# Kernel tuning notes

Measured on AMD Instinct MI355X. Metric: run time of the kernel, lower is better.

Reference implementation:

```python
import jax, jax.numpy as jnp
import numpy as np

B, T, STEPS = 4096, 56, 28
H, ANN, ENC, DEC = 126, 30, 20, 15
DIN = 1 + DEC + H  # decoder GRU input width = 142


def _gru_step(h, x, Wih, Whh, bih, bhh):
    # torch GRU cell math; Wih: [3H, in], Whh: [3H, H]
    gi = x @ Wih.T + bih
    gh = h @ Whh.T + bhh
    ir, iz, inn = jnp.split(gi, 3, axis=-1)
    hr, hz, hn = jnp.split(gh, 3, axis=-1)
    r = jax.nn.sigmoid(ir + hr)
    z = jax.nn.sigmoid(iz + hz)
    n = jnp.tanh(inn + r * hn)
    return (1.0 - z) * n + z * h


def setup_inputs() -> dict:
    key = jax.random.key(0)
    ks = jax.random.split(key, 23)
    p = lambda k, s: jax.random.normal(k, s, dtype=jnp.float32) * 0.08
    return {
        "ann_data": jax.random.normal(ks[0], (B, ANN), dtype=jnp.float32),
        "encoder_data": jax.random.normal(ks[1], (T, B, ENC), dtype=jnp.float32),
        "decoder_data": jax.random.normal(ks[2], (STEPS, B, DEC), dtype=jnp.float32),
        "s2h_W1": p(ks[3], (96, ANN)), "s2h_b1": p(ks[4], (96,)),
        "s2h_W2": p(ks[5], (H, 96)), "s2h_b2": p(ks[6], (H,)),
        "enc_Wih": p(ks[7], (3 * H, ENC)), "enc_Whh": p(ks[8], (3 * H, H)),
        "enc_bih": p(ks[9], (3 * H,)), "enc_bhh": p(ks[10], (3 * H,)),
        "dec_Wih": p(ks[11], (3 * H, DIN)), "dec_Whh": p(ks[12], (3 * H, H)),
        "dec_bih": p(ks[13], (3 * H,)), "dec_bhh": p(ks[14], (3 * H,)),
        "U_W": p(ks[15], (H, H)), "U_b": p(ks[16], (H,)),
        "Wl_W": p(ks[17], (H, H)), "Wl_b": p(ks[18], (H,)),
        "V_W": p(ks[19], (1, H)), "V_b": p(ks[20], (1,)),
        "h2o_W": p(ks[21], (1, H)), "h2o_b": p(ks[22], (1,)),
    }


def reference(ann_data, encoder_data, decoder_data,
              s2h_W1, s2h_b1, s2h_W2, s2h_b2,
              enc_Wih, enc_Whh, enc_bih, enc_bhh,
              dec_Wih, dec_Whh, dec_bih, dec_bhh,
              U_W, U_b, Wl_W, Wl_b, V_W, V_b, h2o_W, h2o_b):
    # static -> initial hidden: Linear(ANN,96) -> ReLU -> Linear(96,H)
    hidden = jnp.maximum(ann_data @ s2h_W1.T + s2h_b1, 0.0) @ s2h_W2.T + s2h_b2  # [B,H]

    def enc_f(h, x):
        h2 = _gru_step(h, x, enc_Wih, enc_Whh, enc_bih, enc_bhh)
        return h2, h2

    hidden, enc_out = jax.lax.scan(enc_f, hidden, encoder_data)  # enc_out: [T,B,H]

    Uo = enc_out @ U_W.T + U_b            # [T,B,H] precomputed (loop-invariant)
    gt0 = encoder_data[-1, :, 0:1]        # initial_ground, [B,1]

    def dec_f(carry, dec_x):
        h, prev = carry
        Wh = h @ Wl_W.T + Wl_b                              # [B,H]
        scores = jnp.tanh(Uo + Wh[None]) @ V_W.T + V_b      # [T,B,1]
        alpha = jax.nn.softmax(scores, axis=0)              # softmax over time
        attn = jnp.einsum('tb,tbh->bh', alpha[..., 0], enc_out)
        x = jnp.concatenate([prev, dec_x, attn], axis=1)    # [B,DIN]
        h2 = _gru_step(h, x, dec_Wih, dec_Whh, dec_bih, dec_bhh)
        out = h2 @ h2o_W.T + h2o_b                          # [B,1]
        return (h2, out), out

    _, outputs = jax.lax.scan(dec_f, (hidden, gt0), decoder_data)
    return outputs  # [STEPS, B, 1]
```

## Files before the change

kernel.cpp:

```cpp
#include <hip/hip_runtime.h>
#include <stdint.h>

typedef unsigned int u32;
typedef unsigned short u16;
typedef _Float16 f16;
typedef _Float16 f16x8 __attribute__((ext_vector_type(8)));
typedef _Float16 f16x4 __attribute__((ext_vector_type(4)));
typedef _Float16 f16x2 __attribute__((ext_vector_type(2)));
typedef float f32x4 __attribute__((ext_vector_type(4)));

constexpr int NB = 4096;
constexpr int NT = 56;
constexpr int NS = 28;
constexpr int NH = 126;
constexpr int NHP = 128;
constexpr float LOG2E = 1.4426950408889634f;

constexpr int LROW = 136;
constexpr int LB   = NT * LROW + 8;

constexpr int TJP = 120;
constexpr int TB  = 7712;

constexpr size_t OFF_H    = 0;
constexpr size_t OFF_ENC  = 2097152;
constexpr size_t OFF_UO   = OFF_ENC + 58720256;
constexpr size_t OFF_WENC = OFF_UO + 58720256;
constexpr size_t OFF_WDEC = OFF_WENC + 122880;
constexpr size_t OFF_WL   = OFF_WDEC + 221184;
constexpr size_t OFF_UW   = OFF_WL + 32768;

__device__ __forceinline__ float fexp2(float x){ return __builtin_amdgcn_exp2f(x); }
__device__ __forceinline__ float frcp (float x){ return __builtin_amdgcn_rcpf(x); }
__device__ __forceinline__ float sigm (float x){ return frcp(1.f + fexp2(-LOG2E * x)); }
__device__ __forceinline__ float ftanh(float x){ return 1.f - 2.f * frcp(1.f + fexp2(2.f * LOG2E * x)); }

__global__ void k_prep(const float* __restrict__ eWih, const float* __restrict__ eWhh,
                       const float* __restrict__ dWih, const float* __restrict__ dWhh,
                       const float* __restrict__ UW,   const float* __restrict__ Wl,
                       char* __restrict__ ws)
{
  f16* wenc = (f16*)(ws + OFF_WENC);
  f16* wdec = (f16*)(ws + OFF_WDEC);
  f16* wl   = (f16*)(ws + OFF_WL);
  f16* uw   = (f16*)(ws + OFF_UW);
  const int nE = 384 * 160, nD = 384 * 288, nW = 128 * 128;
  const int total = nE + nD + nW + nW;
  for (int i = blockIdx.x * 256 + threadIdx.x; i < total; i += gridDim.x * 256) {
    int idx = i;
    if (idx < nE) {
      const int r = idx / 160, c = idx % 160;
      float v = 0.f;
      if (r < 378) {
        if (c < 20) v = eWih[r * 20 + c];
        else if (c >= 32 && c < 158) v = eWhh[r * 126 + (c - 32)];
      }
      wenc[idx] = (f16)v; continue;
    }
    idx -= nE;
    if (idx < nD) {
      const int r = idx / 288, c = idx % 288;
      float v = 0.f;
      if (r < 378) {
        if (c < 16) v = dWih[r * 142 + c];
        else if (c >= 32 && c < 158) v = dWih[r * 142 + 16 + (c - 32)];
        else if (c >= 160 && c < 286) v = dWhh[r * 126 + (c - 160)];
      }
      wdec[idx] = (f16)v; continue;
    }
    idx -= nD;
    if (idx < nW) {
      const int r = idx >> 7, c = idx & 127;
      wl[idx] = (f16)((r < 126 && c < 126) ? Wl[r * 126 + c] : 0.f);
      continue;
    }
    idx -= nW;
    { const int r = idx >> 7, c = idx & 127;
      uw[idx] = (f16)((r < 126 && c < 126) ? UW[r * 126 + c] : 0.f); }
  }
}

__global__ __launch_bounds__(256) void k_mlp(
    const float* __restrict__ ann, const float* __restrict__ W1, const float* __restrict__ b1,
    const float* __restrict__ W2, const float* __restrict__ b2, float* __restrict__ hstate)
{
  __shared__ float anns[32][33];
  __shared__ float t1s[32][101];
  const int tid = threadIdx.x;
  const int b0 = blockIdx.x * 32;
  for (int i = tid; i < 32 * 30; i += 256)
    anns[i / 30][i % 30] = ann[(b0 + i / 30) * 30 + (i % 30)];
  __syncthreads();
  const int b = tid & 31, rg = tid >> 5;
  for (int m = rg; m < 96; m += 8) {
    float a = b1[m];
    for (int k = 0; k < 30; ++k) a += W1[m * 30 + k] * anns[b][k];
    t1s[b][m] = fmaxf(a, 0.f);
  }
  __syncthreads();
  for (int j = rg; j < NHP; j += 8) {
    float a = 0.f;
    if (j < NH) {
      a = b2[j];
      for (int k = 0; k < 96; ++k) a += W2[j * 96 + k] * t1s[b][k];
    }
    hstate[(b0 + b) * NHP + j] = a;
  }
}

__global__ __launch_bounds__(512) void k_enc(
    const float* __restrict__ xenc, const f16* __restrict__ Wenc,
    const f16* __restrict__ Uw,
    const float* __restrict__ bih, const float* __restrict__ bhh,
    const float* __restrict__ Ub,
    float* __restrict__ hstate, f16* __restrict__ encO, u16* __restrict__ uoO)
{
  __shared__ f16 av[16][296];
  const int tid = threadIdx.x;
  const int wid = tid >> 6, l = tid & 63, quad = l >> 4, col = l & 15;
  const int b0 = blockIdx.x * 16;
  const int jb = wid * 16, j = jb + col;
  const bool valid = j < NH;
  const int jc = valid ? j : NH - 1;

  const float br  = bih[jc]        + bhh[jc];
  const float bz  = bih[NH + jc]   + bhh[NH + jc];
  const float bnx = bih[2*NH + jc];
  const float bnh = bhh[2*NH + jc];
  const float ub  = Ub[jc];

  f16x8 rB[5], zB[5], nxB, nhB[4], uB[4];
  {
    const int ko = quad * 8, rr = jb + col;
#pragma unroll
    for (int kt = 0; kt < 5; ++kt) {
      rB[kt] = *(const f16x8*)&Wenc[rr * 160 + kt * 32 + ko];
      zB[kt] = *(const f16x8*)&Wenc[(NH + rr) * 160 + kt * 32 + ko];
    }
    nxB = *(const f16x8*)&Wenc[(2*NH + rr) * 160 + ko];
#pragma unroll
    for (int kt = 0; kt < 4; ++kt) {
      nhB[kt] = *(const f16x8*)&Wenc[(2*NH + rr) * 160 + 32 + kt * 32 + ko];
      uB[kt]  = *(const f16x8*)&Uw[rr * 128 + kt * 32 + ko];
    }
  }

  {
    const int bb = tid >> 5, c4 = (tid & 31) * 4;
    const float4 hv = *(const float4*)&hstate[(b0 + bb) * NHP + c4];
    av[bb][32 + c4]     = (f16)hv.x; av[bb][32 + c4 + 1] = (f16)hv.y;
    av[bb][32 + c4 + 2] = (f16)hv.z; av[bb][32 + c4 + 3] = (f16)hv.w;
  }
  if (tid < 192) { const int bb = tid / 12, p = tid % 12; av[bb][20 + p] = (f16)0.f; }
  __syncthreads();

  const int m = col, ko = quad * 8;
  for (int t = 0; t < NT; ++t) {
    const int hp = 32 + (t & 1) * 128, hq = 32 + ((t + 1) & 1) * 128;
    if (tid < 320) {
      const int bb = tid / 20, e = tid % 20;
      av[bb][e] = (f16)xenc[((size_t)t * NB + b0 + bb) * 20 + e];
    }
    __syncthreads();
    f16x8 A[5];
    A[0] = *(const f16x8*)&av[m][ko];
#pragma unroll
    for (int kt = 1; kt < 5; ++kt) A[kt] = *(const f16x8*)&av[m][hp + (kt - 1) * 32 + ko];

    f32x4 Cr = {br, br, br, br}, Cz = {bz, bz, bz, bz};
    f32x4 Cnx = {bnx, bnx, bnx, bnx}, Cnh = {bnh, bnh, bnh, bnh};
#pragma unroll
    for (int kt = 0; kt < 5; ++kt) {
      Cr = __builtin_amdgcn_mfma_f32_16x16x32_f16(A[kt], rB[kt], Cr, 0, 0, 0);
      Cz = __builtin_amdgcn_mfma_f32_16x16x32_f16(A[kt], zB[kt], Cz, 0, 0, 0);
    }
    Cnx = __builtin_amdgcn_mfma_f32_16x16x32_f16(A[0], nxB, Cnx, 0, 0, 0);
#pragma unroll
    for (int kt = 0; kt < 4; ++kt)
      Cnh = __builtin_amdgcn_mfma_f32_16x16x32_f16(A[kt + 1], nhB[kt], Cnh, 0, 0, 0);

    float hv4[4];
#pragma unroll
    for (int c = 0; c < 4; ++c) {
      const int bb = quad * 4 + c;
      const float hold = (float)av[bb][hp + j];
      const float r = sigm(Cr[c]), z = sigm(Cz[c]);
      const float n = ftanh(Cnx[c] + r * Cnh[c]);
      hv4[c] = (1.f - z) * n + z * hold;
    }
#pragma unroll
    for (int c = 0; c < 4; ++c) {
      const int bb = quad * 4 + c;
      const f16 hs = valid ? (f16)hv4[c] : (f16)0.f;
      av[bb][hq + j] = hs;
      encO[((size_t)(b0 + bb) * NT + t) * 128 + j] = hs;
    }
    if (t == NT - 1 && valid) {
#pragma unroll
      for (int c = 0; c < 4; ++c)
        hstate[(b0 + quad * 4 + c) * NHP + j] = hv4[c];
    }
    __syncthreads();

    f16x8 Ah[4];
#pragma unroll
    for (int kt = 0; kt < 4; ++kt) Ah[kt] = *(const f16x8*)&av[m][hq + kt * 32 + ko];
    f32x4 Cu = {ub, ub, ub, ub};
#pragma unroll
    for (int kt = 0; kt < 4; ++kt)
      Cu = __builtin_amdgcn_mfma_f32_16x16x32_f16(Ah[kt], uB[kt], Cu, 0, 0, 0);
#pragma unroll
    for (int c = 0; c < 4; ++c) {
      union { f16 h; u16 u; } cv;
      cv.h = (f16)fexp2(2.f * LOG2E * Cu[c]);
      uoO[((size_t)(b0 + quad * 4 + c) * NT + t) * 128 + j] = valid ? cv.u : (u16)0;
    }
  }
}

__global__ __launch_bounds__(512, 2) void k_dec(
    const float* __restrict__ xdec, const float* __restrict__ xenc,
    const f16* __restrict__ Wdec, const f16* __restrict__ WlW,
    const float* __restrict__ bih, const float* __restrict__ bhh,
    const float* __restrict__ Wlb, const float* __restrict__ Vw,
    const float* __restrict__ Vb, const float* __restrict__ how,
    const float* __restrict__ hob, const float* __restrict__ hstate,
    const f16* __restrict__ encO, const u16* __restrict__ uoO,
    float* __restrict__ out)
{
  __shared__ __align__(16) u16 uoL[4 * LB];
  __shared__ __align__(16) f16 encT[4 * TB];
  __shared__ __align__(16) f16 av[5][424];
  __shared__ float EWS[4][132];
  __shared__ float scS[4][60];
  __shared__ __align__(16) f16 hows16[128];
  const int tid = threadIdx.x;
  const int wid = tid >> 6, l = tid & 63, quad = l >> 4, col = l & 15;
  const int b0 = blockIdx.x * 4;
  const int jb = wid * 16, j = jb + col;
  const bool valid = j < NH;
  const int jc = valid ? j : NH - 1;

  const float br  = bih[jc]        + bhh[jc];
  const float bz  = bih[NH + jc]   + bhh[NH + jc];
  const float bnx = bih[2*NH + jc];
  const float bnh = bhh[2*NH + jc];
  const float wb  = Wlb[jc];
  const float vb0 = Vb[0], hob0 = hob[0];

  f16x8 rB[9], zB[9], nxB[5], nhB[4], wlB[4];
  {
    const int ko = quad * 8, rr = jb + col;
#pragma unroll
    for (int kt = 0; kt < 9; ++kt) {
      rB[kt] = *(const f16x8*)&Wdec[rr * 288 + kt * 32 + ko];
      zB[kt] = *(const f16x8*)&Wdec[(NH + rr) * 288 + kt * 32 + ko];
    }
#pragma unroll
    for (int kt = 0; kt < 5; ++kt)
      nxB[kt] = *(const f16x8*)&Wdec[(2*NH + rr) * 288 + kt * 32 + ko];
#pragma unroll
    for (int kt = 0; kt < 4; ++kt) {
      nhB[kt] = *(const f16x8*)&Wdec[(2*NH + rr) * 288 + 160 + kt * 32 + ko];
      wlB[kt] = *(const f16x8*)&WlW[rr * 128 + kt * 32 + ko];
    }
  }

  const int g = tid >> 3, sub = tid & 7;
  float n2v[16], svsum = 0.f;
#pragma unroll
  for (int i = 0; i < 16; ++i) {
    const int jj = sub * 16 + i;
    const float v = (jj < NH) ? Vw[jj] : 0.f;
    n2v[i] = -2.f * v;
    svsum += v;
  }
  if (tid >= 256 && tid < 384) {
    const int q = tid - 256; hows16[q] = (f16)((q < NH) ? how[q] : 0.f);
  }
  for (int i = tid; i < 5 * 424; i += 512) av[i / 424][i % 424] = (f16)0.f;
  if (tid < 24) EWS[tid / 6][126 + tid % 6] = 0.f;
  {
    const size_t gb = (size_t)b0 * NT * 128;
    for (int i = tid; i < 4 * NT * 16; i += 512) {
      const int ch = i & 15, btr = i >> 4;
      const int bb = btr / NT, tt = btr % NT;
      const size_t src = gb + (size_t)btr * 128 + ch * 8;
      *(f16x8*)&uoL[bb * LB + tt * LROW + ch * 8] = *(const f16x8*)&uoO[src];
      const f16x8 ev = *(const f16x8*)&encO[src];
#pragma unroll
      for (int k2 = 0; k2 < 4; ++k2) {
        f16x2 pr; pr[0] = ev[2 * k2]; pr[1] = ev[2 * k2 + 1];
        *(f16x2*)&encT[bb * TB + (ch * 4 + k2) * TJP + tt * 2] = pr;
      }
    }
  }
  __syncthreads();
  if (tid < 128) {
    const int bb = tid >> 5, c4 = (tid & 31) * 4;
    const float4 hv = *(const float4*)&hstate[(b0 + bb) * NHP + c4];
    av[bb][160 + c4]     = (f16)hv.x; av[bb][160 + c4 + 1] = (f16)hv.y;
    av[bb][160 + c4 + 2] = (f16)hv.z; av[bb][160 + c4 + 3] = (f16)hv.w;
  }
  if (tid < 4) av[tid][0] = (f16)xenc[((size_t)(NT - 1) * NB + b0 + tid) * 20];
  __syncthreads();

  const int m = col, ko = quad * 8;
  const int arow = ((m & 3) == 0) ? (m >> 2) : 4;
  const int pb = tid & 3, pth = (tid >> 2) & 1, pjp = tid >> 3;

  for (int s = 0; s < NS; ++s) {
    const int hp = 160 + (s & 1) * 128, hq = 160 + ((s + 1) & 1) * 128;

    {
      f16x8 Ah[4];
#pragma unroll
      for (int kt = 0; kt < 4; ++kt) Ah[kt] = *(const f16x8*)&av[arow][hp + kt * 32 + ko];
      f32x4 Cw = {wb, wb, wb, wb};
#pragma unroll
      for (int kt = 0; kt < 4; ++kt)
        Cw = __builtin_amdgcn_mfma_f32_16x16x32_f16(Ah[kt], wlB[kt], Cw, 0, 0, 0);
      if (valid) EWS[quad][j] = fexp2(2.f * LOG2E * Cw[0]);
      if (wid == 0 && s > 0) {
        f16x8 hB[4];
        const f16x8 zz = {};
#pragma unroll
        for (int kt = 0; kt < 4; ++kt)
          hB[kt] = (col == 0) ? *(const f16x8*)&hows16[kt * 32 + ko] : zz;
        f32x4 Co = {0.f, 0.f, 0.f, 0.f};
#pragma unroll
        for (int kt = 0; kt < 4; ++kt)
          Co = __builtin_amdgcn_mfma_f32_16x16x32_f16(Ah[kt], hB[kt], Co, 0, 0, 0);
        if (col == 0) {
          const float o = Co[0] + hob0;
          out[(size_t)(s - 1) * NB + b0 + quad] = o;
          av[quad][0] = (f16)o;
        }
      }
    }
    if (tid < 60) { const int bb = tid / 15, e = tid % 15;
      av[bb][1 + e] = (f16)xdec[((size_t)s * NB + b0 + bb) * 15 + e]; }
    __syncthreads();

    {
      const int sbb = g & 3, tb = g >> 2;
      float ew[16];
#pragma unroll
      for (int i = 0; i < 4; ++i)
        *(float4*)&ew[i * 4] = *(const float4*)&EWS[sbb][sub * 16 + i * 4];
      const u16* up0 = &uoL[sbb * LB + sub * 16];
      uint4 q0 = *(const uint4*)&up0[tb * LROW];
      uint4 q1 = *(const uint4*)&up0[tb * LROW + 8];
      float rs[4];
#pragma unroll
      for (int rd = 0; rd < 4; ++rd) {
        const int t = rd * 16 + tb;
        const u32 wsv[8] = {q0.x, q0.y, q0.z, q0.w, q1.x, q1.y, q1.z, q1.w};
        if (rd < 3) {
          const int tn = (t + 16 < NT) ? (t + 16) : (NT - 1);
          q0 = *(const uint4*)&up0[tn * LROW];
          q1 = *(const uint4*)&up0[tn * LROW + 8];
        }
        float ac0 = 0.f, ac1 = 0.f, ac2 = 0.f, ac3 = 0.f;
#pragma unroll
        for (int k = 0; k < 8; k += 2) {
          union { u32 i; f16x2 h; } ua, ub2;
          ua.i = wsv[k]; ub2.i = wsv[k + 1];
          const float p0 = fmaf((float)ua.h[0],  ew[2 * k],     1.f);
          const float p1 = fmaf((float)ua.h[1],  ew[2 * k + 1], 1.f);
          const float p2 = fmaf((float)ub2.h[0], ew[2 * k + 2], 1.f);
          const float p3 = fmaf((float)ub2.h[1], ew[2 * k + 3], 1.f);
          ac0 = fmaf(n2v[2 * k],     frcp(p0), ac0);
          ac1 = fmaf(n2v[2 * k + 1], frcp(p1), ac1);
          ac2 = fmaf(n2v[2 * k + 2], frcp(p2), ac2);
          ac3 = fmaf(n2v[2 * k + 3], frcp(p3), ac3);
        }
        rs[rd] = svsum + (ac0 + ac1) + (ac2 + ac3);
      }
      rs[0] += __shfl_xor(rs[0], 1, 64);
      rs[1] += __shfl_xor(rs[1], 1, 64);
      rs[2] += __shfl_xor(rs[2], 1, 64);
      rs[3] += __shfl_xor(rs[3], 1, 64);
      rs[0] += __shfl_xor(rs[0], 2, 64);
      rs[1] += __shfl_xor(rs[1], 2, 64);
      rs[2] += __shfl_xor(rs[2], 2, 64);
      rs[3] += __shfl_xor(rs[3], 2, 64);
      rs[0] += __shfl_xor(rs[0], 4, 64);
      rs[1] += __shfl_xor(rs[1], 4, 64);
      rs[2] += __shfl_xor(rs[2], 4, 64);
      rs[3] += __shfl_xor(rs[3], 4, 64);
      if (sub == 0) {
#pragma unroll
        for (int rd = 0; rd < 4; ++rd) {
          const int t = rd * 16 + tb;
          if (t < NT) scS[sbb][t] = fexp2(LOG2E * (rs[rd] + vb0));
        }
      }
    }
    __syncthreads();

    {
      const int j0 = pjp * 2;
      const f16* er = &encT[pb * TB + pjp * TJP + pth * 56];
      const float* scp = &scS[pb][pth * 28];
      float Za = 0.f, Zb = 0.f;
      float a0a = 0.f, a0b = 0.f, a1a = 0.f, a1b = 0.f;
#pragma unroll
      for (int it = 0; it < 7; ++it) {
        const f16x8 ev = *(const f16x8*)&er[it * 8];
        const float4 sc = *(const float4*)&scp[it * 4];
        Za += sc.x; Zb += sc.y; Za += sc.z; Zb += sc.w;
        a0a = fmaf(sc.x, (float)ev[0], a0a);
        a1a = fmaf(sc.x, (float)ev[1], a1a);
        a0b = fmaf(sc.y, (float)ev[2], a0b);
        a1b = fmaf(sc.y, (float)ev[3], a1b);
        a0a = fmaf(sc.z, (float)ev[4], a0a);
        a1a = fmaf(sc.z, (float)ev[5], a1a);
        a0b = fmaf(sc.w, (float)ev[6], a0b);
        a1b = fmaf(sc.w, (float)ev[7], a1b);
      }
      float Z = Za + Zb, a0 = a0a + a0b, a1 = a1a + a1b;
      a0 += __shfl_xor(a0, 4, 64);
      a1 += __shfl_xor(a1, 4, 64);
      Z  += __shfl_xor(Z, 4, 64);
      if (pth == 0) {
        const float inv = frcp(Z);
        f16x2 st; st[0] = (f16)(a0 * inv); st[1] = (f16)(a1 * inv);
        *(f16x2*)&av[pb][32 + j0] = st;
      }
    }
    __syncthreads();

    {
      f16x8 A[9];
#pragma unroll
      for (int kt = 0; kt < 5; ++kt) A[kt] = *(const f16x8*)&av[arow][kt * 32 + ko];
#pragma unroll
      for (int kt = 5; kt < 9; ++kt) A[kt] = *(const f16x8*)&av[arow][hp + (kt - 5) * 32 + ko];
      f32x4 Cr = {br, br, br, br}, Cz = {bz, bz, bz, bz};
      f32x4 Cnx = {bnx, bnx, bnx, bnx}, Cnh = {bnh, bnh, bnh, bnh};
#pragma unroll
      for (int kt = 0; kt < 9; ++kt) {
        Cr = __builtin_amdgcn_mfma_f32_16x16x32_f16(A[kt], rB[kt], Cr, 0, 0, 0);
        Cz = __builtin_amdgcn_mfma_f32_16x16x32_f16(A[kt], zB[kt], Cz, 0, 0, 0);
      }
#pragma unroll
      for (int kt = 0; kt < 5; ++kt)
        Cnx = __builtin_amdgcn_mfma_f32_16x16x32_f16(A[kt], nxB[kt], Cnx, 0, 0, 0);
#pragma unroll
      for (int kt = 0; kt < 4; ++kt)
        Cnh = __builtin_amdgcn_mfma_f32_16x16x32_f16(A[kt + 5], nhB[kt], Cnh, 0, 0, 0);
      {
        const float hold = (float)av[quad][hp + j];
        const float r = sigm(Cr[0]), z = sigm(Cz[0]);
        const float n = ftanh(Cnx[0] + r * Cnh[0]);
        const float h2 = (1.f - z) * n + z * hold;
        if (valid) av[quad][hq + j] = (f16)h2;
      }
    }
    __syncthreads();
  }

  if (wid == 0) {
    const int hql = 160 + (NS & 1) * 128;
    f16x8 Ah2[4], hB[4];
    const f16x8 zz = {};
#pragma unroll
    for (int kt = 0; kt < 4; ++kt) {
      Ah2[kt] = *(const f16x8*)&av[arow][hql + kt * 32 + ko];
      hB[kt] = (col == 0) ? *(const f16x8*)&hows16[kt * 32 + ko] : zz;
    }
    f32x4 Co = {0.f, 0.f, 0.f, 0.f};
#pragma unroll
    for (int kt = 0; kt < 4; ++kt)
      Co = __builtin_amdgcn_mfma_f32_16x16x32_f16(Ah2[kt], hB[kt], Co, 0, 0, 0);
    if (col == 0) out[(size_t)(NS - 1) * NB + b0 + quad] = Co[0] + hob0;
  }
}

extern "C" void kernel_launch(void* const* d_in, const int* in_sizes, int n_in,
                              void* d_out, int out_size, void* d_ws, size_t ws_size,
                              hipStream_t stream)
{
  const float* ann   = (const float*)d_in[0];
  const float* xenc  = (const float*)d_in[1];
  const float* xdec  = (const float*)d_in[2];
  const float* W1    = (const float*)d_in[3];
  const float* b1    = (const float*)d_in[4];
  const float* W2    = (const float*)d_in[5];
  const float* b2    = (const float*)d_in[6];
  const float* eWih  = (const float*)d_in[7];
  const float* eWhh  = (const float*)d_in[8];
  const float* ebih  = (const float*)d_in[9];
  const float* ebhh  = (const float*)d_in[10];
  const float* dWih  = (const float*)d_in[11];
  const float* dWhh  = (const float*)d_in[12];
  const float* dbih  = (const float*)d_in[13];
  const float* dbhh  = (const float*)d_in[14];
  const float* UW    = (const float*)d_in[15];
  const float* Ubias = (const float*)d_in[16];
  const float* Wl    = (const float*)d_in[17];
  const float* Wlb   = (const float*)d_in[18];
  const float* Vw    = (const float*)d_in[19];
  const float* Vb    = (const float*)d_in[20];
  const float* how   = (const float*)d_in[21];
  const float* hob   = (const float*)d_in[22];

  char* ws = (char*)d_ws;
  float* hstate = (float*)(ws + OFF_H);
  f16*   encB   = (f16*)(ws + OFF_ENC);
  u16*   uoB    = (u16*)(ws + OFF_UO);
  const f16* pWenc = (const f16*)(ws + OFF_WENC);
  const f16* pWdec = (const f16*)(ws + OFF_WDEC);
  const f16* pWl   = (const f16*)(ws + OFF_WL);
  const f16* pUW   = (const f16*)(ws + OFF_UW);

  k_prep<<<200, 256, 0, stream>>>(eWih, eWhh, dWih, dWhh, UW, Wl, ws);
  k_mlp <<<128, 256, 0, stream>>>(ann, W1, b1, W2, b2, hstate);
  k_enc <<<NB / 16, 512, 0, stream>>>(xenc, pWenc, pUW, ebih, ebhh, Ubias,
                                      hstate, encB, uoB);
  k_dec <<<NB / 4, 512, 0, stream>>>(xdec, xenc, pWdec, pWl, dbih, dbhh,
                                     Wlb, Vw, Vb, how, hob, hstate,
                                     encB, uoB, (float*)d_out);
}
```

Before: 584.7 us.

## Compute attention context with MFMA over j-major transposed encoder outputs

Replaces the scalar FMA loop that builds the attention context vector with MFMA 16x16x32 f16 instructions. Encoder outputs are stored j-major in LDS with zero-padded time columns. The softmax weights are also written as f16 so they can serve as the B operand, and the normalizer is reduced with lane shuffles. Only column 0 of each MFMA output is used, so most of the matrix work is wasted. Rounding the softmax weights to f16 costs some accuracy, and the byte-wise transposed LDS stores in the prologue may cause bank conflicts.

```diff
diff --git a/kernel.cpp b/kernel.cpp
--- a/kernel.cpp
+++ b/kernel.cpp
@@ -19,8 +19,8 @@
 constexpr int LROW = 136;
 constexpr int LB   = NT * LROW + 8;
 
-constexpr int TJP = 120;
-constexpr int TB  = 7712;
+constexpr int ETROW = 72;
+constexpr int ETB   = 128 * ETROW;
 
 constexpr size_t OFF_H    = 0;
 constexpr size_t OFF_ENC  = 2097152;
@@ -229,10 +229,11 @@
     float* __restrict__ out)
 {
   __shared__ __align__(16) u16 uoL[4 * LB];
-  __shared__ __align__(16) f16 encT[4 * TB];
+  __shared__ __align__(16) f16 encTj[4 * ETB];
   __shared__ __align__(16) f16 av[5][424];
   __shared__ float EWS[4][132];
-  __shared__ float scS[4][60];
+  __shared__ __align__(16) float scS[4][68];
+  __shared__ __align__(16) f16 scSf16[5][72];
   __shared__ __align__(16) f16 hows16[128];
   const int tid = threadIdx.x;
   const int wid = tid >> 6, l = tid & 63, quad = l >> 4, col = l & 15;
@@ -280,6 +281,13 @@
   }
   for (int i = tid; i < 5 * 424; i += 512) av[i / 424][i % 424] = (f16)0.f;
   if (tid < 24) EWS[tid / 6][126 + tid % 6] = 0.f;
+  for (int i = tid; i < 4 * 68; i += 512) (&scS[0][0])[i] = 0.f;
+  for (int i = tid; i < 5 * 72; i += 512) (&scSf16[0][0])[i] = (f16)0.f;
+  {
+    const f16x8 zz = {};
+    *(f16x8*)&encTj[tid * ETROW + 56] = zz;
+    *(f16x8*)&encTj[tid * ETROW + 64] = zz;
+  }
   {
     const size_t gb = (size_t)b0 * NT * 128;
     for (int i = tid; i < 4 * NT * 16; i += 512) {
@@ -289,10 +297,8 @@
       *(f16x8*)&uoL[bb * LB + tt * LROW + ch * 8] = *(const f16x8*)&uoO[src];
       const f16x8 ev = *(const f16x8*)&encO[src];
 #pragma unroll
-      for (int k2 = 0; k2 < 4; ++k2) {
-        f16x2 pr; pr[0] = ev[2 * k2]; pr[1] = ev[2 * k2 + 1];
-        *(f16x2*)&encT[bb * TB + (ch * 4 + k2) * TJP + tt * 2] = pr;
-      }
+      for (int k2 = 0; k2 < 8; ++k2)
+        encTj[bb * ETB + (ch * 8 + k2) * ETROW + tt] = ev[k2];
     }
   }
   __syncthreads();
@@ -307,7 +313,6 @@
 
   const int m = col, ko = quad * 8;
   const int arow = ((m & 3) == 0) ? (m >> 2) : 4;
-  const int pb = tid & 3, pth = (tid >> 2) & 1, pjp = tid >> 3;
 
   for (int s = 0; s < NS; ++s) {
     const int hp = 160 + (s & 1) * 128, hq = 160 + ((s + 1) & 1) * 128;
@@ -393,40 +398,42 @@
 #pragma unroll
         for (int rd = 0; rd < 4; ++rd) {
           const int t = rd * 16 + tb;
-          if (t < NT) scS[sbb][t] = fexp2(LOG2E * (rs[rd] + vb0));
+          if (t < NT) {
+            const float ex = fexp2(LOG2E * (rs[rd] + vb0));
+            scS[sbb][t] = ex;
+            scSf16[sbb][t] = (f16)ex;
+          }
         }
       }
     }
     __syncthreads();
 
     {
-      const int j0 = pjp * 2;
-      const f16* er = &encT[pb * TB + pjp * TJP + pth * 56];
-      const float* scp = &scS[pb][pth * 28];
-      float Za = 0.f, Zb = 0.f;
-      float a0a = 0.f, a0b = 0.f, a1a = 0.f, a1b = 0.f;
-#pragma unroll
-      for (int it = 0; it < 7; ++it) {
-        const f16x8 ev = *(const f16x8*)&er[it * 8];
-        const float4 sc = *(const float4*)&scp[it * 4];
-        Za += sc.x; Zb += sc.y; Za += sc.z; Zb += sc.w;
-        a0a = fmaf(sc.x, (float)ev[0], a0a);
-        a1a = fmaf(sc.x, (float)ev[1], a1a);
-        a0b = fmaf(sc.y, (float)ev[2], a0b);
-        a1b = fmaf(sc.y, (float)ev[3], a1b);
-        a0a = fmaf(sc.z, (float)ev[4], a0a);
-        a1a = fmaf(sc.z, (float)ev[5], a1a);
-        a0b = fmaf(sc.w, (float)ev[6], a0b);
-        a1b = fmaf(sc.w, (float)ev[7], a1b);
-      }
-      float Z = Za + Zb, a0 = a0a + a0b, a1 = a1a + a1b;
-      a0 += __shfl_xor(a0, 4, 64);
-      a1 += __shfl_xor(a1, 4, 64);
-      Z  += __shfl_xor(Z, 4, 64);
-      if (pth == 0) {
-        const float inv = frcp(Z);
-        f16x2 st; st[0] = (f16)(a0 * inv); st[1] = (f16)(a1 * inv);
-        *(f16x2*)&av[pb][32 + j0] = st;
+      const float4 zv = *(const float4*)&scS[quad][col * 4];
+      float Zp = (zv.x + zv.y) + (zv.z + zv.w);
+      Zp += __shfl_xor(Zp, 1, 64);
+      Zp += __shfl_xor(Zp, 2, 64);
+      Zp += __shfl_xor(Zp, 4, 64);
+      Zp += __shfl_xor(Zp, 8, 64);
+      const float invZq = frcp(Zp);
+#pragma unroll
+      for (int b = 0; b < 4; ++b) {
+        const float ivb = __shfl(invZq, b * 16 + col, 64);
+        const f16* ar = &encTj[b * ETB + (jb + col) * ETROW];
+        const f16x8 A0 = *(const f16x8*)&ar[ko];
+        const f16x8 A1 = *(const f16x8*)&ar[32 + ko];
+        const int rbat = (col == 0) ? b : 4;
+        const f16x8 B0 = *(const f16x8*)&scSf16[rbat][ko];
+        const f16x8 B1 = *(const f16x8*)&scSf16[rbat][32 + ko];
+        f32x4 Ca = {0.f, 0.f, 0.f, 0.f};
+        Ca = __builtin_amdgcn_mfma_f32_16x16x32_f16(A0, B0, Ca, 0, 0, 0);
+        Ca = __builtin_amdgcn_mfma_f32_16x16x32_f16(A1, B1, Ca, 0, 0, 0);
+        if (col == 0) {
+          f16x4 st;
+#pragma unroll
+          for (int r = 0; r < 4; ++r) st[r] = (f16)(Ca[r] * ivb);
+          *(f16x4*)&av[b][32 + jb + quad * 4] = st;
+        }
       }
     }
     __syncthreads();
```

Result: slower. 614.1 us (+5.0%).

## Split decoder GRU matmuls across two wave halves using 1024-thread blocks

Applied to the files above, without the earlier changes.

The decoder kernel doubles its block to 1024 threads. The two halves of the waves split the GRU gate work: one half computes the input-side projections for r, z and n, the other computes the hidden-side projections and the Wl attention query. Partial sums pass through new shared arrays with an extra barrier. The attention score and context loops are also re-split so each thread handles fewer timesteps, and n2v moves into shared memory. The goal is to shorten the serial per-step critical path and cut register pressure, at the cost of more barriers, more shared memory and possibly lower occupancy.

```diff
diff --git a/kernel.cpp b/kernel.cpp
--- a/kernel.cpp
+++ b/kernel.cpp
@@ -218,7 +218,7 @@
   }
 }
 
-__global__ __launch_bounds__(512, 2) void k_dec(
+__global__ __launch_bounds__(1024, 4) void k_dec(
     const float* __restrict__ xdec, const float* __restrict__ xenc,
     const f16* __restrict__ Wdec, const f16* __restrict__ WlW,
     const float* __restrict__ bih, const float* __restrict__ bhh,
@@ -233,11 +233,14 @@
   __shared__ __align__(16) f16 av[5][424];
   __shared__ float EWS[4][132];
   __shared__ float scS[4][60];
+  __shared__ float pxr[4][132], pxz[4][132], pxn[4][132];
+  __shared__ float n2vL[128];
   __shared__ __align__(16) f16 hows16[128];
   const int tid = threadIdx.x;
   const int wid = tid >> 6, l = tid & 63, quad = l >> 4, col = l & 15;
+  const int kh = wid >> 3, jw = wid & 7;
   const int b0 = blockIdx.x * 4;
-  const int jb = wid * 16, j = jb + col;
+  const int jb = jw * 16, j = jb + col;
   const bool valid = j < NH;
   const int jc = valid ? j : NH - 1;
 
@@ -248,41 +251,44 @@
   const float wb  = Wlb[jc];
   const float vb0 = Vb[0], hob0 = hob[0];
 
-  f16x8 rB[9], zB[9], nxB[5], nhB[4], wlB[4];
+  f16x8 W[16];
   {
     const int ko = quad * 8, rr = jb + col;
-#pragma unroll
-    for (int kt = 0; kt < 9; ++kt) {
-      rB[kt] = *(const f16x8*)&Wdec[rr * 288 + kt * 32 + ko];
-      zB[kt] = *(const f16x8*)&Wdec[(NH + rr) * 288 + kt * 32 + ko];
-    }
-#pragma unroll
-    for (int kt = 0; kt < 5; ++kt)
-      nxB[kt] = *(const f16x8*)&Wdec[(2*NH + rr) * 288 + kt * 32 + ko];
-#pragma unroll
-    for (int kt = 0; kt < 4; ++kt) {
-      nhB[kt] = *(const f16x8*)&Wdec[(2*NH + rr) * 288 + 160 + kt * 32 + ko];
-      wlB[kt] = *(const f16x8*)&WlW[rr * 128 + kt * 32 + ko];
+    if (kh == 0) {
+#pragma unroll
+      for (int kt = 0; kt < 5; ++kt) {
+        W[kt]      = *(const f16x8*)&Wdec[rr * 288 + kt * 32 + ko];
+        W[5 + kt]  = *(const f16x8*)&Wdec[(NH + rr) * 288 + kt * 32 + ko];
+        W[10 + kt] = *(const f16x8*)&Wdec[(2*NH + rr) * 288 + kt * 32 + ko];
+      }
+      W[15] = (f16x8){};
+    } else {
+#pragma unroll
+      for (int kt = 0; kt < 4; ++kt) {
+        W[kt]      = *(const f16x8*)&Wdec[rr * 288 + 160 + kt * 32 + ko];
+        W[4 + kt]  = *(const f16x8*)&Wdec[(NH + rr) * 288 + 160 + kt * 32 + ko];
+        W[8 + kt]  = *(const f16x8*)&Wdec[(2*NH + rr) * 288 + 160 + kt * 32 + ko];
+        W[12 + kt] = *(const f16x8*)&WlW[rr * 128 + kt * 32 + ko];
+      }
     }
   }
 
   const int g = tid >> 3, sub = tid & 7;
-  float n2v[16], svsum = 0.f;
+  float svsum = 0.f;
 #pragma unroll
   for (int i = 0; i < 16; ++i) {
     const int jj = sub * 16 + i;
-    const float v = (jj < NH) ? Vw[jj] : 0.f;
-    n2v[i] = -2.f * v;
-    svsum += v;
-  }
+    svsum += (jj < NH) ? Vw[jj] : 0.f;
+  }
+  if (tid < 128) n2vL[tid] = -2.f * ((tid < NH) ? Vw[tid] : 0.f);
   if (tid >= 256 && tid < 384) {
     const int q = tid - 256; hows16[q] = (f16)((q < NH) ? how[q] : 0.f);
   }
-  for (int i = tid; i < 5 * 424; i += 512) av[i / 424][i % 424] = (f16)0.f;
+  for (int i = tid; i < 5 * 424; i += 1024) av[i / 424][i % 424] = (f16)0.f;
   if (tid < 24) EWS[tid / 6][126 + tid % 6] = 0.f;
   {
     const size_t gb = (size_t)b0 * NT * 128;
-    for (int i = tid; i < 4 * NT * 16; i += 512) {
+    for (int i = tid; i < 4 * NT * 16; i += 1024) {
       const int ch = i & 15, btr = i >> 4;
       const int bb = btr / NT, tt = btr % NT;
       const size_t src = gb + (size_t)btr * 128 + ch * 8;
@@ -307,21 +313,21 @@
 
   const int m = col, ko = quad * 8;
   const int arow = ((m & 3) == 0) ? (m >> 2) : 4;
-  const int pb = tid & 3, pth = (tid >> 2) & 1, pjp = tid >> 3;
+  const int pb = tid & 3, pth = (tid >> 2) & 3, pjp = tid >> 4;
 
   for (int s = 0; s < NS; ++s) {
     const int hp = 160 + (s & 1) * 128, hq = 160 + ((s + 1) & 1) * 128;
 
-    {
+    if (kh == 1) {
       f16x8 Ah[4];
 #pragma unroll
       for (int kt = 0; kt < 4; ++kt) Ah[kt] = *(const f16x8*)&av[arow][hp + kt * 32 + ko];
       f32x4 Cw = {wb, wb, wb, wb};
 #pragma unroll
       for (int kt = 0; kt < 4; ++kt)
-        Cw = __builtin_amdgcn_mfma_f32_16x16x32_f16(Ah[kt], wlB[kt], Cw, 0, 0, 0);
+        Cw = __builtin_amdgcn_mfma_f32_16x16x32_f16(Ah[kt], W[12 + kt], Cw, 0, 0, 0);
       if (valid) EWS[quad][j] = fexp2(2.f * LOG2E * Cw[0]);
-      if (wid == 0 && s > 0) {
+      if (wid == 8 && s > 0) {
         f16x8 hB[4];
         const f16x8 zz = {};
 #pragma unroll
@@ -344,20 +350,21 @@
 
     {
       const int sbb = g & 3, tb = g >> 2;
-      float ew[16];
-#pragma unroll
-      for (int i = 0; i < 4; ++i)
+      float ew[16], nv[16];
+#pragma unroll
+      for (int i = 0; i < 4; ++i) {
         *(float4*)&ew[i * 4] = *(const float4*)&EWS[sbb][sub * 16 + i * 4];
+        *(float4*)&nv[i * 4] = *(const float4*)&n2vL[sub * 16 + i * 4];
+      }
       const u16* up0 = &uoL[sbb * LB + sub * 16];
       uint4 q0 = *(const uint4*)&up0[tb * LROW];
       uint4 q1 = *(const uint4*)&up0[tb * LROW + 8];
-      float rs[4];
-#pragma unroll
-      for (int rd = 0; rd < 4; ++rd) {
-        const int t = rd * 16 + tb;
+      float rs[2];
+#pragma unroll
+      for (int rd = 0; rd < 2; ++rd) {
         const u32 wsv[8] = {q0.x, q0.y, q0.z, q0.w, q1.x, q1.y, q1.z, q1.w};
-        if (rd < 3) {
-          const int tn = (t + 16 < NT) ? (t + 16) : (NT - 1);
+        if (rd == 0) {
+          const int tn = (32 + tb < NT) ? (32 + tb) : (NT - 1);
           q0 = *(const uint4*)&up0[tn * LROW];
           q1 = *(const uint4*)&up0[tn * LROW + 8];
         }
@@ -370,59 +377,56 @@
           const float p1 = fmaf((float)ua.h[1],  ew[2 * k + 1], 1.f);
           const float p2 = fmaf((float)ub2.h[0], ew[2 * k + 2], 1.f);
           const float p3 = fmaf((float)ub2.h[1], ew[2 * k + 3], 1.f);
-          ac0 = fmaf(n2v[2 * k],     frcp(p0), ac0);
-          ac1 = fmaf(n2v[2 * k + 1], frcp(p1), ac1);
-          ac2 = fmaf(n2v[2 * k + 2], frcp(p2), ac2);
-          ac3 = fmaf(n2v[2 * k + 3], frcp(p3), ac3);
+          ac0 = fmaf(nv[2 * k],     frcp(p0), ac0);
+          ac1 = fmaf(nv[2 * k + 1], frcp(p1), ac1);
+          ac2 = fmaf(nv[2 * k + 2], frcp(p2), ac2);
+          ac3 = fmaf(nv[2 * k + 3], frcp(p3), ac3);
         }
         rs[rd] = svsum + (ac0 + ac1) + (ac2 + ac3);
       }
       rs[0] += __shfl_xor(rs[0], 1, 64);
       rs[1] += __shfl_xor(rs[1], 1, 64);
-      rs[2] += __shfl_xor(rs[2], 1, 64);
-      rs[3] += __shfl_xor(rs[3], 1, 64);
       rs[0] += __shfl_xor(rs[0], 2, 64);
       rs[1] += __shfl_xor(rs[1], 2, 64);
-      rs[2] += __shfl_xor(rs[2], 2, 64);
-      rs[3] += __shfl_xor(rs[3], 2, 64);
       rs[0] += __shfl_xor(rs[0], 4, 64);
       rs[1] += __shfl_xor(rs[1], 4, 64);
-      rs[2] += __shfl_xor(rs[2], 4, 64);
-      rs[3] += __shfl_xor(rs[3], 4, 64);
       if (sub == 0) {
-#pragma unroll
-        for (int rd = 0; rd < 4; ++rd) {
-          const int t = rd * 16 + tb;
-          if (t < NT) scS[sbb][t] = fexp2(LOG2E * (rs[rd] + vb0));
-        }
+        scS[sbb][tb] = fexp2(LOG2E * (rs[0] + vb0));
+        if (32 + tb < NT) scS[sbb][32 + tb] = fexp2(LOG2E * (rs[1] + vb0));
       }
     }
     __syncthreads();
 
     {
       const int j0 = pjp * 2;
-      const f16* er = &encT[pb * TB + pjp * TJP + pth * 56];
-      const float* scp = &scS[pb][pth * 28];
+      const f16* er = &encT[pb * TB + pjp * TJP + pth * 32];
+      const float* scp = &scS[pb][pth * 16];
+      const int nit = (pth == 3) ? 2 : 4;
       float Za = 0.f, Zb = 0.f;
       float a0a = 0.f, a0b = 0.f, a1a = 0.f, a1b = 0.f;
 #pragma unroll
-      for (int it = 0; it < 7; ++it) {
-        const f16x8 ev = *(const f16x8*)&er[it * 8];
-        const float4 sc = *(const float4*)&scp[it * 4];
-        Za += sc.x; Zb += sc.y; Za += sc.z; Zb += sc.w;
-        a0a = fmaf(sc.x, (float)ev[0], a0a);
-        a1a = fmaf(sc.x, (float)ev[1], a1a);
-        a0b = fmaf(sc.y, (float)ev[2], a0b);
-        a1b = fmaf(sc.y, (float)ev[3], a1b);
-        a0a = fmaf(sc.z, (float)ev[4], a0a);
-        a1a = fmaf(sc.z, (float)ev[5], a1a);
-        a0b = fmaf(sc.w, (float)ev[6], a0b);
-        a1b = fmaf(sc.w, (float)ev[7], a1b);
+      for (int it = 0; it < 4; ++it) {
+        if (it < nit) {
+          const f16x8 ev = *(const f16x8*)&er[it * 8];
+          const float4 sc = *(const float4*)&scp[it * 4];
+          Za += sc.x + sc.z; Zb += sc.y + sc.w;
+          a0a = fmaf(sc.x, (float)ev[0], a0a);
+          a1a = fmaf(sc.x, (float)ev[1], a1a);
+          a0b = fmaf(sc.y, (float)ev[2], a0b);
+          a1b = fmaf(sc.y, (float)ev[3], a1b);
+          a0a = fmaf(sc.z, (float)ev[4], a0a);
+          a1a = fmaf(sc.z, (float)ev[5], a1a);
+          a0b = fmaf(sc.w, (float)ev[6], a0b);
+          a1b = fmaf(sc.w, (float)ev[7], a1b);
+        }
       }
       float Z = Za + Zb, a0 = a0a + a0b, a1 = a1a + a1b;
       a0 += __shfl_xor(a0, 4, 64);
       a1 += __shfl_xor(a1, 4, 64);
       Z  += __shfl_xor(Z, 4, 64);
+      a0 += __shfl_xor(a0, 8, 64);
+      a1 += __shfl_xor(a1, 8, 64);
+      Z  += __shfl_xor(Z, 8, 64);
       if (pth == 0) {
         const float inv = frcp(Z);
         f16x2 st; st[0] = (f16)(a0 * inv); st[1] = (f16)(a1 * inv);
@@ -431,37 +435,46 @@
     }
     __syncthreads();
 
-    {
-      f16x8 A[9];
+    if (kh == 0) {
+      f16x8 A[5];
 #pragma unroll
       for (int kt = 0; kt < 5; ++kt) A[kt] = *(const f16x8*)&av[arow][kt * 32 + ko];
-#pragma unroll
-      for (int kt = 5; kt < 9; ++kt) A[kt] = *(const f16x8*)&av[arow][hp + (kt - 5) * 32 + ko];
       f32x4 Cr = {br, br, br, br}, Cz = {bz, bz, bz, bz};
-      f32x4 Cnx = {bnx, bnx, bnx, bnx}, Cnh = {bnh, bnh, bnh, bnh};
-#pragma unroll
-      for (int kt = 0; kt < 9; ++kt) {
-        Cr = __builtin_amdgcn_mfma_f32_16x16x32_f16(A[kt], rB[kt], Cr, 0, 0, 0);
-        Cz = __builtin_amdgcn_mfma_f32_16x16x32_f16(A[kt], zB[kt], Cz, 0, 0, 0);
-      }
-#pragma unroll
-      for (int kt = 0; kt < 5; ++kt)
-        Cnx = __builtin_amdgcn_mfma_f32_16x16x32_f16(A[kt], nxB[kt], Cnx, 0, 0, 0);
-#pragma unroll
-      for (int kt = 0; kt < 4; ++kt)
-        Cnh = __builtin_amdgcn_mfma_f32_16x16x32_f16(A[kt + 5], nhB[kt], Cnh, 0, 0, 0);
-      {
-        const float hold = (float)av[quad][hp + j];
-        const float r = sigm(Cr[0]), z = sigm(Cz[0]);
-        const float n = ftanh(Cnx[0] + r * Cnh[0]);
-        const float h2 = (1.f - z) * n + z * hold;
-        if (valid) av[quad][hq + j] = (f16)h2;
-      }
+      f32x4 Cnx = {bnx, bnx, bnx, bnx};
+#pragma unroll
+      for (int kt = 0; kt < 5; ++kt) {
+        Cr  = __builtin_amdgcn_mfma_f32_16x16x32_f16(A[kt], W[kt],      Cr,  0, 0, 0);
+        Cz  = __builtin_amdgcn_mfma_f32_16x16x32_f16(A[kt], W[5 + kt],  Cz,  0, 0, 0);
+        Cnx = __builtin_amdgcn_mfma_f32_16x16x32_f16(A[kt], W[10 + kt], Cnx, 0, 0, 0);
+      }
+      pxr[quad][j] = Cr[0];
+      pxz[quad][j] = Cz[0];
+      pxn[quad][j] = Cnx[0];
+      __syncthreads();
+    } else {
+      f16x8 Ah[4];
+#pragma unroll
+      for (int kt = 0; kt < 4; ++kt) Ah[kt] = *(const f16x8*)&av[arow][hp + kt * 32 + ko];
+      f32x4 Cr = {0.f, 0.f, 0.f, 0.f}, Cz = {0.f, 0.f, 0.f, 0.f};
+      f32x4 Cnh = {bnh, bnh, bnh, bnh};
+#pragma unroll
+      for (int kt = 0; kt < 4; ++kt) {
+        Cr  = __builtin_amdgcn_mfma_f32_16x16x32_f16(Ah[kt], W[kt],     Cr,  0, 0, 0);
+        Cz  = __builtin_amdgcn_mfma_f32_16x16x32_f16(Ah[kt], W[4 + kt], Cz,  0, 0, 0);
+        Cnh = __builtin_amdgcn_mfma_f32_16x16x32_f16(Ah[kt], W[8 + kt], Cnh, 0, 0, 0);
+      }
+      __syncthreads();
+      const float hold = (float)av[quad][hp + j];
+      const float r = sigm(pxr[quad][j] + Cr[0]);
+      const float z = sigm(pxz[quad][j] + Cz[0]);
+      const float n = ftanh(pxn[quad][j] + r * Cnh[0]);
+      const float h2 = (1.f - z) * n + z * hold;
+      if (valid) av[quad][hq + j] = (f16)h2;
     }
     __syncthreads();
   }
 
-  if (wid == 0) {
+  if (wid == 8) {
     const int hql = 160 + (NS & 1) * 128;
     f16x8 Ah2[4], hB[4];
     const f16x8 zz = {};
@@ -519,7 +532,7 @@
   k_mlp <<<128, 256, 0, stream>>>(ann, W1, b1, W2, b2, hstate);
   k_enc <<<NB / 16, 512, 0, stream>>>(xenc, pWenc, pUW, ebih, ebhh, Ubias,
                                       hstate, encB, uoB);
-  k_dec <<<NB / 4, 512, 0, stream>>>(xdec, xenc, pWdec, pWl, dbih, dbhh,
-                                     Wlb, Vw, Vb, how, hob, hstate,
-                                     encB, uoB, (float*)d_out);
+  k_dec <<<NB / 4, 1024, 0, stream>>>(xdec, xenc, pWdec, pWl, dbih, dbhh,
+                                      Wlb, Vw, Vb, how, hob, hstate,
+                                      encB, uoB, (float*)d_out);
 }
```

After: 1.099 ms. 1.88x slower.

## Software-pipeline encoder loop: prefetch next input, defer U projection, drop barrier

Applied to the files above, without the earlier changes.

The encoder loop now loads the next timestep's input into a register and double-buffers it in shared memory. This removes one of the two __syncthreads per step and hides the global-load latency. The U-projection MFMA for step t-1 is moved into step t, reusing the A fragments of the previous hidden state already loaded for the GRU. A tail block handles the final step. The cost is more shared memory per row and slightly more live registers.

```diff
diff --git a/kernel.cpp b/kernel.cpp
--- a/kernel.cpp
+++ b/kernel.cpp
@@ -21,6 +21,8 @@
 
 constexpr int TJP = 120;
 constexpr int TB  = 7712;
+
+constexpr int EROW = 344;
 
 constexpr size_t OFF_H    = 0;
 constexpr size_t OFF_ENC  = 2097152;
@@ -115,7 +117,7 @@
     const float* __restrict__ Ub,
     float* __restrict__ hstate, f16* __restrict__ encO, u16* __restrict__ uoO)
 {
-  __shared__ f16 av[16][296];
+  __shared__ f16 av[16][EROW];
   const int tid = threadIdx.x;
   const int wid = tid >> 6, l = tid & 63, quad = l >> 4, col = l & 15;
   const int b0 = blockIdx.x * 16;
@@ -151,21 +153,41 @@
     av[bb][32 + c4]     = (f16)hv.x; av[bb][32 + c4 + 1] = (f16)hv.y;
     av[bb][32 + c4 + 2] = (f16)hv.z; av[bb][32 + c4 + 3] = (f16)hv.w;
   }
-  if (tid < 192) { const int bb = tid / 12, p = tid % 12; av[bb][20 + p] = (f16)0.f; }
+  if (tid < 384) {
+    const int bb = tid / 24, p = tid % 24;
+    av[bb][(p < 12) ? (20 + p) : (312 + p)] = (f16)0.f;
+  }
+  const int bb320 = tid / 20, e320 = tid % 20;
+  if (tid < 320)
+    av[bb320][e320] = (f16)xenc[((size_t)0 * NB + b0 + bb320) * 20 + e320];
   __syncthreads();
 
   const int m = col, ko = quad * 8;
   for (int t = 0; t < NT; ++t) {
     const int hp = 32 + (t & 1) * 128, hq = 32 + ((t + 1) & 1) * 128;
-    if (tid < 320) {
-      const int bb = tid / 20, e = tid % 20;
-      av[bb][e] = (f16)xenc[((size_t)t * NB + b0 + bb) * 20 + e];
-    }
-    __syncthreads();
+    const int xp = (t & 1) ? 304 : 0,  xq = ((t + 1) & 1) ? 304 : 0;
+
+    float xv = 0.f;
+    const bool ldx = (tid < 320) && (t + 1 < NT);
+    if (ldx) xv = xenc[((size_t)(t + 1) * NB + b0 + bb320) * 20 + e320];
+
     f16x8 A[5];
-    A[0] = *(const f16x8*)&av[m][ko];
+    A[0] = *(const f16x8*)&av[m][xp + ko];
 #pragma unroll
     for (int kt = 1; kt < 5; ++kt) A[kt] = *(const f16x8*)&av[m][hp + (kt - 1) * 32 + ko];
+
+    if (t) {
+      f32x4 Cu = {ub, ub, ub, ub};
+#pragma unroll
+      for (int kt = 0; kt < 4; ++kt)
+        Cu = __builtin_amdgcn_mfma_f32_16x16x32_f16(A[kt + 1], uB[kt], Cu, 0, 0, 0);
+#pragma unroll
+      for (int c = 0; c < 4; ++c) {
+        union { f16 h; u16 u; } cv;
+        cv.h = (f16)fexp2(2.f * LOG2E * Cu[c]);
+        uoO[((size_t)(b0 + quad * 4 + c) * NT + (t - 1)) * 128 + j] = valid ? cv.u : (u16)0;
+      }
+    }
 
     f32x4 Cr = {br, br, br, br}, Cz = {bz, bz, bz, bz};
     f32x4 Cnx = {bnx, bnx, bnx, bnx}, Cnh = {bnh, bnh, bnh, bnh};
@@ -200,11 +222,14 @@
       for (int c = 0; c < 4; ++c)
         hstate[(b0 + quad * 4 + c) * NHP + j] = hv4[c];
     }
+    if (ldx) av[bb320][xq + e320] = (f16)xv;
     __syncthreads();
-
+  }
+
+  {
     f16x8 Ah[4];
 #pragma unroll
-    for (int kt = 0; kt < 4; ++kt) Ah[kt] = *(const f16x8*)&av[m][hq + kt * 32 + ko];
+    for (int kt = 0; kt < 4; ++kt) Ah[kt] = *(const f16x8*)&av[m][32 + kt * 32 + ko];
     f32x4 Cu = {ub, ub, ub, ub};
 #pragma unroll
     for (int kt = 0; kt < 4; ++kt)
@@ -213,7 +238,7 @@
     for (int c = 0; c < 4; ++c) {
       union { f16 h; u16 u; } cv;
       cv.h = (f16)fexp2(2.f * LOG2E * Cu[c]);
-      uoO[((size_t)(b0 + quad * 4 + c) * NT + t) * 128 + j] = valid ? cv.u : (u16)0;
+      uoO[((size_t)(b0 + quad * 4 + c) * NT + (NT - 1)) * 128 + j] = valid ? cv.u : (u16)0;
     }
   }
 }
```

Result: no change. 582.3 us (-0.4%).
